# Optimization experiments

Hardware: AMD Instinct MI355X
Metric: run time of the kernel (lower is better)

Reference implementation:

```python
import jax, jax.numpy as jnp
import numpy as np

BLOCK_SIZE = 16
NVFP4_LEVELS = np.array([0.0, 0.5, 1.0, 1.5, 2.0, 3.0, 4.0, 6.0], dtype=np.float32)


def quantize_to_nvfp4(x, block_size=BLOCK_SIZE):
    """NVFP4 fake-quant: per-16-element block, scale = amax/6, round |x| to nearest level."""
    levels = jnp.asarray(NVFP4_LEVELS, dtype=x.dtype)
    orig_shape = x.shape
    xf = x.reshape(-1, block_size)                                   # [nblk, 16]
    amax = jnp.clip(jnp.max(jnp.abs(xf), axis=-1, keepdims=True), 1e-12)
    scale = amax / 6.0                                               # [nblk, 1]
    x_norm = jnp.abs(xf) / scale                                     # in [0, 6]
    idx = jnp.argmin(jnp.abs(x_norm[..., None] - levels), axis=-1)   # nearest level (first on ties, like torch)
    x_q = jnp.sign(xf) * levels[idx] * scale
    return x_q.reshape(orig_shape)


def _magnitude_mask_2_4(w):
    # keep 2 largest-|.| of every group of 4 along in_features (row-wise 2:4)
    out_f, in_f = w.shape
    a = jnp.abs(w).reshape(out_f, in_f // 4, 4)
    thr = jnp.sort(a, axis=-1)[..., 2:3]          # 2nd-largest magnitude in group
    mask = (a >= thr).reshape(out_f, in_f)
    return mask.astype(w.dtype)


def setup_inputs() -> dict:
    key = jax.random.key(0)
    k_x, k_w, k_s, k_a, k_b, k_bias = jax.random.split(key, 6)
    B, S, IN_F, OUT_F, RANK = 2, 2048, 4096, 4096, 32
    x = jax.random.normal(k_x, (B, S, IN_F), dtype=jnp.float32)
    smooth_scale = jax.random.uniform(k_s, (IN_F,), dtype=jnp.float32, minval=0.5, maxval=2.0)
    # realistic calibrated weight: 2:4 magnitude-sparse then NVFP4 fake-quantized
    w = jax.random.normal(k_w, (OUT_F, IN_F), dtype=jnp.float32) * 0.02
    w_sparse = w * _magnitude_mask_2_4(w)
    w_quantized = quantize_to_nvfp4(w_sparse)
    lora_a = jax.random.normal(k_a, (RANK, IN_F), dtype=jnp.float32) * 0.02
    lora_b = jax.random.normal(k_b, (OUT_F, RANK), dtype=jnp.float32) * 0.02
    bias = jax.random.normal(k_bias, (OUT_F,), dtype=jnp.float32)
    return {"x": x, "smooth_scale": smooth_scale, "w_quantized": w_quantized,
            "lora_a": lora_a, "lora_b": lora_b, "bias": bias}


def reference(x, smooth_scale, w_quantized, lora_a, lora_b, bias):
    # x: [B, S, IN], smooth_scale: [IN], w_quantized: [OUT, IN]
    x_smoothed = x * smooth_scale                                    # SmoothQuant activation scaling
    x_q = quantize_to_nvfp4(x_smoothed, BLOCK_SIZE)                  # block fake-quant of activations
    base_out = jnp.einsum('bsi,oi->bso', x_q, w_quantized)           # 2:4-sparse quantized matmul
    svd_out = jnp.einsum('bsr,or->bso',
                         jnp.einsum('bsi,ri->bsr', x_smoothed, lora_a), lora_b)  # low-rank correction
    return base_out + svd_out + bias
```

## Files before the change

### kernel.cpp

```cpp
#include <hip/hip_runtime.h>
#include <hip/hip_bf16.h>
#include <stdint.h>

typedef __attribute__((ext_vector_type(8))) __bf16 bf16x8;
typedef __attribute__((ext_vector_type(4))) float f32x4;

#define KP 4160

__device__ inline void async_copy16(const void* g, void* l) {
  __builtin_amdgcn_global_load_lds((const __attribute__((address_space(1))) void*)g,
                                   (__attribute__((address_space(3))) void*)l, 16, 0, 0);
}

__global__ __launch_bounds__(256) void fused_quant_lora_kernel(
    const float* __restrict__ x, const float* __restrict__ ss,
    const float* __restrict__ la, __bf16* __restrict__ Ab,
    float* __restrict__ Tp) {
  __shared__ float red[4][16][32];
  int tid  = threadIdx.x;
  int m0   = blockIdx.x << 4;
  int by   = blockIdx.y;

  {
    int row = m0 + (tid >> 4);
    int cb0 = tid & 15;
#pragma unroll
    for (int i = 0; i < 4; i++) {
      int col = (by << 10) + ((cb0 + (i << 4)) << 4);
      const float4* xp = (const float4*)(x + ((size_t)row << 12) + col);
      const float4* sp = (const float4*)(ss + col);
      float xs[16];
#pragma unroll
      for (int j = 0; j < 4; j++) {
        float4 xv = xp[j]; float4 sv = sp[j];
        xs[4*j+0] = xv.x * sv.x; xs[4*j+1] = xv.y * sv.y;
        xs[4*j+2] = xv.z * sv.z; xs[4*j+3] = xv.w * sv.w;
      }
      float amax = 0.f;
#pragma unroll
      for (int j = 0; j < 16; j++) amax = fmaxf(amax, fabsf(xs[j]));
      amax = fmaxf(amax, 1e-12f);
      float scale = amax / 6.0f;
      bf16x8 o0, o1;
#pragma unroll
      for (int j = 0; j < 16; j++) {
        float a  = fabsf(xs[j]);
        float xn = a / scale;
        float bestd = xn;
        float lvl   = 0.f;
        const float L[7] = {0.5f, 1.f, 1.5f, 2.f, 3.f, 4.f, 6.f};
#pragma unroll
        for (int l = 0; l < 7; l++) {
          float d = fabsf(xn - L[l]);
          if (d < bestd) { bestd = d; lvl = L[l]; }
        }
        float mag = lvl * scale;
        float q = (xs[j] > 0.f) ? mag : ((xs[j] < 0.f) ? -mag : 0.f);
        if (j < 8) o0[j] = (__bf16)q; else o1[j-8] = (__bf16)q;
      }
      __bf16* dst = Ab + (size_t)row * KP + col;
      *(bf16x8*)dst = o0;
      *(bf16x8*)(dst + 8) = o1;
    }
  }

  {
    int wave = tid >> 6, lane = tid & 63;
    int lrow = lane & 15, kg = lane >> 4;
    int kbase = (by << 10) + (wave << 8);
    f32x4 acc0 = {0.f,0.f,0.f,0.f}, acc1 = {0.f,0.f,0.f,0.f};
    const float* xrow = x + ((size_t)(m0 + lrow) << 12);
    const float* a0   = la + ((size_t)lrow << 12);
    const float* a1   = a0 + (16 << 12);
#pragma unroll
    for (int k0 = 0; k0 < 256; k0 += 32) {
      int kk = kbase + k0 + (kg << 3);
      float xv[8], sv[8], v0[8], v1[8];
      *(float4*)&xv[0] = *(const float4*)(xrow + kk);
      *(float4*)&xv[4] = *(const float4*)(xrow + kk + 4);
      *(float4*)&sv[0] = *(const float4*)(ss + kk);
      *(float4*)&sv[4] = *(const float4*)(ss + kk + 4);
      *(float4*)&v0[0] = *(const float4*)(a0 + kk);
      *(float4*)&v0[4] = *(const float4*)(a0 + kk + 4);
      *(float4*)&v1[0] = *(const float4*)(a1 + kk);
      *(float4*)&v1[4] = *(const float4*)(a1 + kk + 4);
      bf16x8 af, b0, b1;
#pragma unroll
      for (int j = 0; j < 8; j++) {
        af[j] = (__bf16)(xv[j] * sv[j]);
        b0[j] = (__bf16)v0[j];
        b1[j] = (__bf16)v1[j];
      }
      acc0 = __builtin_amdgcn_mfma_f32_16x16x32_bf16(af, b0, acc0, 0, 0, 0);
      acc1 = __builtin_amdgcn_mfma_f32_16x16x32_bf16(af, b1, acc1, 0, 0, 0);
    }
#pragma unroll
    for (int r = 0; r < 4; r++) {
      red[wave][kg*4 + r][lrow]      = acc0[r];
      red[wave][kg*4 + r][16 + lrow] = acc1[r];
    }
    __syncthreads();
    for (int o = tid; o < 512; o += 256) {
      int rr = o >> 5, cc = o & 31;
      float s = red[0][rr][cc] + red[1][rr][cc] + red[2][rr][cc] + red[3][rr][cc];
      Tp[((size_t)by * 4096 + m0 + rr) * 32 + cc] = s;
    }
  }
}

__global__ __launch_bounds__(256) void lora_fix_kernel(const float* __restrict__ Tp,
                                                       __bf16* __restrict__ Ab) {
  int id  = blockIdx.x * 256 + threadIdx.x;
  int row = id >> 5, cc = id & 31;
  float s = 0.f;
#pragma unroll
  for (int kc = 0; kc < 4; kc++)
    s += Tp[((size_t)kc * 4096 + row) * 32 + cc];
  __bf16* dst = Ab + (size_t)row * KP + 4096;
  dst[cc]      = (__bf16)s;
  dst[32 + cc] = (__bf16)0.f;
}

__global__ __launch_bounds__(256) void wconv_kernel(const float* __restrict__ w,
                                                    const float* __restrict__ lb,
                                                    __bf16* __restrict__ Bb) {
  int id  = blockIdx.x * 256 + threadIdx.x;
  int row = id / 520;
  int g   = id - row * 520;
  bf16x8 v;
  if (g < 512) {
    const float4* wp = (const float4*)(w + ((size_t)row << 12) + (g << 3));
    float4 a = wp[0], b = wp[1];
    v[0]=(__bf16)a.x; v[1]=(__bf16)a.y; v[2]=(__bf16)a.z; v[3]=(__bf16)a.w;
    v[4]=(__bf16)b.x; v[5]=(__bf16)b.y; v[6]=(__bf16)b.z; v[7]=(__bf16)b.w;
  } else if (g < 516) {
    const float* p = lb + (size_t)row * 32 + ((g - 512) << 3);
#pragma unroll
    for (int j = 0; j < 8; j++) v[j] = (__bf16)p[j];
  } else {
#pragma unroll
    for (int j = 0; j < 8; j++) v[j] = (__bf16)0.f;
  }
  *(bf16x8*)(Bb + (size_t)row * KP + ((size_t)g << 3)) = v;
}

__global__ __launch_bounds__(256) void gemm_kernel(const __bf16* __restrict__ A,
                                                   const __bf16* __restrict__ B,
                                                   const float* __restrict__ bias,
                                                   float* __restrict__ C) {
  __shared__ __bf16 As[128 * 64];
  __shared__ __bf16 Bs[128 * 64];
  int tid  = threadIdx.x;
  int wave = tid >> 6, lane = tid & 63;
  int bm = blockIdx.x >> 5, bn = blockIdx.x & 31;
  size_t m0 = (size_t)bm << 7, n0 = (size_t)bn << 7;
  int wm = wave >> 1, wn = wave & 1;
  int lrow = lane & 15, kg = lane >> 4;
  int srow = lane >> 3;
  int sk   = ((lane & 7) ^ srow) << 3;
  f32x4 acc[4][4];
#pragma unroll
  for (int r = 0; r < 4; r++)
#pragma unroll
    for (int c = 0; c < 4; c++) acc[r][c] = (f32x4){0.f,0.f,0.f,0.f};

  for (int k = 0; k < KP; k += 64) {
#pragma unroll
    for (int i = 0; i < 4; i++) {
      int chunk = (wave << 2) + i;
      int row   = (chunk << 3) + srow;
      async_copy16(A + (m0 + row) * (size_t)KP + k + sk, (void*)(As + chunk * 512));
      async_copy16(B + (n0 + row) * (size_t)KP + k + sk, (void*)(Bs + chunk * 512));
    }
    __syncthreads();
#pragma unroll
    for (int ks = 0; ks < 2; ks++) {
      bf16x8 af[4], bfr[4];
      int kx = ((ks << 6) + (kg << 4)) ^ ((lrow & 7) << 4);
#pragma unroll
      for (int r = 0; r < 4; r++) {
        int ml = (wm << 6) + (r << 4) + lrow;
        af[r]  = *(const bf16x8*)((const char*)As + ml * 128 + kx);
        int nl = (wn << 6) + (r << 4) + lrow;
        bfr[r] = *(const bf16x8*)((const char*)Bs + nl * 128 + kx);
      }
#pragma unroll
      for (int r = 0; r < 4; r++)
#pragma unroll
        for (int c = 0; c < 4; c++)
          acc[r][c] = __builtin_amdgcn_mfma_f32_16x16x32_bf16(af[r], bfr[c], acc[r][c], 0, 0, 0);
    }
    __syncthreads();
  }
#pragma unroll
  for (int c = 0; c < 4; c++) {
    int col = (int)n0 + (wn << 6) + (c << 4) + lrow;
    float bv = bias[col];
#pragma unroll
    for (int r = 0; r < 4; r++) {
      size_t rowb = m0 + (wm << 6) + (r << 4) + (kg << 2);
#pragma unroll
      for (int q = 0; q < 4; q++)
        C[(rowb + q) * 4096 + col] = acc[r][c][q] + bv;
    }
  }
}

extern "C" void kernel_launch(void* const* d_in, const int* in_sizes, int n_in,
                              void* d_out, int out_size, void* d_ws, size_t ws_size,
                              hipStream_t stream) {
  const float* x    = (const float*)d_in[0];
  const float* ss   = (const float*)d_in[1];
  const float* w    = (const float*)d_in[2];
  const float* la   = (const float*)d_in[3];
  const float* lb   = (const float*)d_in[4];
  const float* bias = (const float*)d_in[5];
  float* out = (float*)d_out;

  __bf16* Ab = (__bf16*)d_ws;
  __bf16* Bb = Ab + (size_t)4096 * KP;
  float* Tp = (float*)Bb;

  fused_quant_lora_kernel<<<dim3(256, 4), 256, 0, stream>>>(x, ss, la, Ab, Tp);
  lora_fix_kernel<<<512, 256, 0, stream>>>(Tp, Ab);
  wconv_kernel<<<8320, 256, 0, stream>>>(w, lb, Bb);
  gemm_kernel<<<1024, 256, 0, stream>>>(Ab, Bb, bias, out);
}
```

Baseline: 354.2 us.

## Switch GEMM to 32x32x16 MFMA and merge weight-convert with LoRA fix kernel

The GEMM inner loop now uses 32x32x16 bf16 MFMA tiles (2x2 per wave) in place of 16x16x32 (4x4), which means fewer LDS fragment loads per MFMA and a different accumulator layout in the epilogue. The separate lora_fix and wconv kernels are merged into one launch, and the LoRA partial sums are staged in the output buffer, so Tp no longer aliases Bb and the fix can run in the same launch as the conversion. This saves one kernel launch and improves operand reuse, at the cost of larger accumulator registers per MFMA.

```diff
diff --git a/kernel.cpp b/kernel.cpp
--- a/kernel.cpp
+++ b/kernel.cpp
@@ -2,8 +2,9 @@
 #include <hip/hip_bf16.h>
 #include <stdint.h>
 
-typedef __attribute__((ext_vector_type(8))) __bf16 bf16x8;
-typedef __attribute__((ext_vector_type(4))) float f32x4;
+typedef __attribute__((ext_vector_type(8)))  __bf16 bf16x8;
+typedef __attribute__((ext_vector_type(4)))  float  f32x4;
+typedef __attribute__((ext_vector_type(16))) float  f32x16;
 
 #define KP 4160
 
@@ -108,40 +109,42 @@
   }
 }
 
-__global__ __launch_bounds__(256) void lora_fix_kernel(const float* __restrict__ Tp,
-                                                       __bf16* __restrict__ Ab) {
-  int id  = blockIdx.x * 256 + threadIdx.x;
-  int row = id >> 5, cc = id & 31;
-  float s = 0.f;
-#pragma unroll
-  for (int kc = 0; kc < 4; kc++)
-    s += Tp[((size_t)kc * 4096 + row) * 32 + cc];
-  __bf16* dst = Ab + (size_t)row * KP + 4096;
-  dst[cc]      = (__bf16)s;
-  dst[32 + cc] = (__bf16)0.f;
-}
-
-__global__ __launch_bounds__(256) void wconv_kernel(const float* __restrict__ w,
-                                                    const float* __restrict__ lb,
-                                                    __bf16* __restrict__ Bb) {
-  int id  = blockIdx.x * 256 + threadIdx.x;
-  int row = id / 520;
-  int g   = id - row * 520;
-  bf16x8 v;
-  if (g < 512) {
-    const float4* wp = (const float4*)(w + ((size_t)row << 12) + (g << 3));
-    float4 a = wp[0], b = wp[1];
-    v[0]=(__bf16)a.x; v[1]=(__bf16)a.y; v[2]=(__bf16)a.z; v[3]=(__bf16)a.w;
-    v[4]=(__bf16)b.x; v[5]=(__bf16)b.y; v[6]=(__bf16)b.z; v[7]=(__bf16)b.w;
-  } else if (g < 516) {
-    const float* p = lb + (size_t)row * 32 + ((g - 512) << 3);
-#pragma unroll
-    for (int j = 0; j < 8; j++) v[j] = (__bf16)p[j];
+__global__ __launch_bounds__(256) void wconv_fix_kernel(const float* __restrict__ w,
+                                                        const float* __restrict__ lb,
+                                                        const float* __restrict__ Tp,
+                                                        __bf16* __restrict__ Bb,
+                                                        __bf16* __restrict__ Ab) {
+  int b = blockIdx.x;
+  if (b < 8320) {
+    int id  = b * 256 + threadIdx.x;
+    int row = id / 520;
+    int g   = id - row * 520;
+    bf16x8 v;
+    if (g < 512) {
+      const float4* wp = (const float4*)(w + ((size_t)row << 12) + (g << 3));
+      float4 a = wp[0], bb = wp[1];
+      v[0]=(__bf16)a.x;  v[1]=(__bf16)a.y;  v[2]=(__bf16)a.z;  v[3]=(__bf16)a.w;
+      v[4]=(__bf16)bb.x; v[5]=(__bf16)bb.y; v[6]=(__bf16)bb.z; v[7]=(__bf16)bb.w;
+    } else if (g < 516) {
+      const float* p = lb + (size_t)row * 32 + ((g - 512) << 3);
+#pragma unroll
+      for (int j = 0; j < 8; j++) v[j] = (__bf16)p[j];
+    } else {
+#pragma unroll
+      for (int j = 0; j < 8; j++) v[j] = (__bf16)0.f;
+    }
+    *(bf16x8*)(Bb + (size_t)row * KP + ((size_t)g << 3)) = v;
   } else {
-#pragma unroll
-    for (int j = 0; j < 8; j++) v[j] = (__bf16)0.f;
-  }
-  *(bf16x8*)(Bb + (size_t)row * KP + ((size_t)g << 3)) = v;
+    int id  = (b - 8320) * 256 + threadIdx.x;
+    int row = id >> 5, cc = id & 31;
+    float s = 0.f;
+#pragma unroll
+    for (int kc = 0; kc < 4; kc++)
+      s += Tp[((size_t)kc * 4096 + row) * 32 + cc];
+    __bf16* dst = Ab + (size_t)row * KP + 4096;
+    dst[cc]      = (__bf16)s;
+    dst[32 + cc] = (__bf16)0.f;
+  }
 }
 
 __global__ __launch_bounds__(256) void gemm_kernel(const __bf16* __restrict__ A,
@@ -155,14 +158,17 @@
   int bm = blockIdx.x >> 5, bn = blockIdx.x & 31;
   size_t m0 = (size_t)bm << 7, n0 = (size_t)bn << 7;
   int wm = wave >> 1, wn = wave & 1;
-  int lrow = lane & 15, kg = lane >> 4;
+  int ln31 = lane & 31, kgrp = lane >> 5;
   int srow = lane >> 3;
   int sk   = ((lane & 7) ^ srow) << 3;
-  f32x4 acc[4][4];
-#pragma unroll
-  for (int r = 0; r < 4; r++)
-#pragma unroll
-    for (int c = 0; c < 4; c++) acc[r][c] = (f32x4){0.f,0.f,0.f,0.f};
+  int swz  = (ln31 & 7) << 4;
+  f32x16 acc[2][2];
+#pragma unroll
+  for (int r = 0; r < 2; r++)
+#pragma unroll
+    for (int c = 0; c < 2; c++)
+#pragma unroll
+      for (int q = 0; q < 16; q++) acc[r][c][q] = 0.f;
 
   for (int k = 0; k < KP; k += 64) {
 #pragma unroll
@@ -174,34 +180,36 @@
     }
     __syncthreads();
 #pragma unroll
-    for (int ks = 0; ks < 2; ks++) {
-      bf16x8 af[4], bfr[4];
-      int kx = ((ks << 6) + (kg << 4)) ^ ((lrow & 7) << 4);
-#pragma unroll
-      for (int r = 0; r < 4; r++) {
-        int ml = (wm << 6) + (r << 4) + lrow;
-        af[r]  = *(const bf16x8*)((const char*)As + ml * 128 + kx);
-        int nl = (wn << 6) + (r << 4) + lrow;
-        bfr[r] = *(const bf16x8*)((const char*)Bs + nl * 128 + kx);
-      }
-#pragma unroll
-      for (int r = 0; r < 4; r++)
-#pragma unroll
-        for (int c = 0; c < 4; c++)
-          acc[r][c] = __builtin_amdgcn_mfma_f32_16x16x32_bf16(af[r], bfr[c], acc[r][c], 0, 0, 0);
+    for (int t = 0; t < 4; t++) {
+      int kx = ((t << 5) + (kgrp << 4)) ^ swz;
+      bf16x8 af[2], bfr[2];
+#pragma unroll
+      for (int h = 0; h < 2; h++) {
+        int arow = (wm << 6) + (h << 5) + ln31;
+        af[h]  = *(const bf16x8*)((const char*)As + arow * 128 + kx);
+        int brow = (wn << 6) + (h << 5) + ln31;
+        bfr[h] = *(const bf16x8*)((const char*)Bs + brow * 128 + kx);
+      }
+#pragma unroll
+      for (int r = 0; r < 2; r++)
+#pragma unroll
+        for (int c = 0; c < 2; c++)
+          acc[r][c] = __builtin_amdgcn_mfma_f32_32x32x16_bf16(af[r], bfr[c], acc[r][c], 0, 0, 0);
     }
     __syncthreads();
   }
 #pragma unroll
-  for (int c = 0; c < 4; c++) {
-    int col = (int)n0 + (wn << 6) + (c << 4) + lrow;
+  for (int c = 0; c < 2; c++) {
+    int col = (int)n0 + (wn << 6) + (c << 5) + ln31;
     float bv = bias[col];
 #pragma unroll
-    for (int r = 0; r < 4; r++) {
-      size_t rowb = m0 + (wm << 6) + (r << 4) + (kg << 2);
-#pragma unroll
-      for (int q = 0; q < 4; q++)
-        C[(rowb + q) * 4096 + col] = acc[r][c][q] + bv;
+    for (int r = 0; r < 2; r++) {
+      size_t rowb = m0 + (wm << 6) + (r << 5) + (kgrp << 2);
+#pragma unroll
+      for (int q = 0; q < 16; q++) {
+        size_t row = rowb + (q & 3) + ((q >> 2) << 3);
+        C[row * 4096 + col] = acc[r][c][q] + bv;
+      }
     }
   }
 }
@@ -219,10 +227,9 @@
 
   __bf16* Ab = (__bf16*)d_ws;
   __bf16* Bb = Ab + (size_t)4096 * KP;
-  float* Tp = (float*)Bb;
+  float* Tp = out;
 
   fused_quant_lora_kernel<<<dim3(256, 4), 256, 0, stream>>>(x, ss, la, Ab, Tp);
-  lora_fix_kernel<<<512, 256, 0, stream>>>(Tp, Ab);
-  wconv_kernel<<<8320, 256, 0, stream>>>(w, lb, Bb);
+  wconv_fix_kernel<<<8832, 256, 0, stream>>>(w, lb, Tp, Bb, Ab);
   gemm_kernel<<<1024, 256, 0, stream>>>(Ab, Bb, bias, out);
 }
```

New measurement: 349.4 us. About the same (-1.3%).
